# Performance work log

Hardware: AMD Instinct MI355X
Metric: run time of the kernel (lower is better)

Reference implementation:

```python
import jax, jax.numpy as jnp
import numpy as np

B, D = 8192, 1024
LABEL_SMOOTHING = 0.1
EPS = 1e-7


def setup_inputs() -> dict:
    key = jax.random.key(0)
    k1, k2 = jax.random.split(key)
    # Poincare-ball points must have norm < 1; scale so ||x|| ~ 0.6
    sign_emb = jax.random.normal(k1, (B, D), dtype=jnp.float32) * 0.02
    text_emb = jax.random.normal(k2, (B, D), dtype=jnp.float32) * 0.02
    log_tau = jnp.float32(0.0)   # nn.Parameter(torch.tensor(0.0))
    margin = jnp.float32(0.3)    # nn.Parameter(torch.tensor(0.3))
    return {"sign_emb": sign_emb, "text_emb": text_emb,
            "log_tau": log_tau, "margin": margin}


def poincare_dist_matrix(x, y):
    # Closed form of PoincareBall(c=1).dist for all pairs, no (B,B,d) intermediate:
    # d(x,y) = arccosh(1 + 2||x-y||^2 / ((1-||x||^2)(1-||y||^2)))
    xx = jnp.sum(x * x, axis=-1)                      # (B,)
    yy = jnp.sum(y * y, axis=-1)                      # (B,)
    xy = jnp.einsum('id,jd->ij', x, y)                # (B,B) Gram matmul
    sq = jnp.maximum(xx[:, None] + yy[None, :] - 2.0 * xy, 0.0)
    denom = jnp.maximum((1.0 - xx)[:, None] * (1.0 - yy)[None, :], EPS)
    arg = 1.0 + 2.0 * sq / denom
    return jnp.arccosh(jnp.maximum(arg, 1.0 + EPS))   # (B,B)


def reference(sign_emb, text_emb, log_tau, margin):
    b = sign_emb.shape[0]
    geo_dist = poincare_dist_matrix(sign_emb, text_emb)           # (B,B)
    tau = jax.nn.sigmoid(log_tau) * 1.99 + 0.01
    is_negative = 1.0 - jnp.eye(b, dtype=geo_dist.dtype)
    scores = -geo_dist / tau + jnp.maximum(margin, 0.0) * is_negative
    # CrossEntropyLoss(label_smoothing) with labels = arange(B)
    logp = jax.nn.log_softmax(scores, axis=-1)
    nll = -jnp.diagonal(logp)                                     # (B,)
    smooth = -jnp.mean(logp, axis=-1)                             # (B,)
    loss = jnp.mean((1.0 - LABEL_SMOOTHING) * nll + LABEL_SMOOTHING * smooth)
    pos_dist = jnp.mean(jnp.diagonal(geo_dist))
    return loss, pos_dist, tau, jnp.maximum(margin, margin)  # margin reported as-is
```

## Files before the change

kernel.cpp:

```cpp
#include <hip/hip_runtime.h>
#include <hip/hip_bf16.h>
#include <stdint.h>

#define BN 8192
#define DK 1024
#define BKT 64
#define NKT (DK / BKT)
#define LSMOOTH 0.1f
#define EPSF 1e-7f
#define LN2F 0.69314718055994531f

typedef float f32x4 __attribute__((ext_vector_type(4)));
typedef int   i32x4 __attribute__((ext_vector_type(4)));

__global__ __launch_bounds__(256) void prep_kernel(
    const float* __restrict__ sign, const float* __restrict__ text,
    uint32_t* __restrict__ Aq, uint32_t* __restrict__ Bq,
    float* __restrict__ xx, float* __restrict__ yy, float* __restrict__ accums) {
  const int b = blockIdx.x;
  const int row = b & (BN - 1);
  const bool isB = b >= BN;
  const float4* src = (const float4*)((isB ? text : sign) + (size_t)row * DK);
  uint32_t* dst = (isB ? Bq : Aq) + (size_t)row * (DK / 4);
  const int t = threadIdx.x;
  if (b == 0 && t < 3) accums[t] = 0.f;
  float4 v = src[t];
  int q0 = __float2int_rn(fminf(fmaxf(v.x * 1024.f, -127.f), 127.f));
  int q1 = __float2int_rn(fminf(fmaxf(v.y * 1024.f, -127.f), 127.f));
  int q2 = __float2int_rn(fminf(fmaxf(v.z * 1024.f, -127.f), 127.f));
  int q3 = __float2int_rn(fminf(fmaxf(v.w * 1024.f, -127.f), 127.f));
  dst[t] = (uint32_t)(q0 & 0xFF) | ((uint32_t)(q1 & 0xFF) << 8) |
           ((uint32_t)(q2 & 0xFF) << 16) | ((uint32_t)(q3 & 0xFF) << 24);
  float ss = v.x * v.x + v.y * v.y + v.z * v.z + v.w * v.w;
  #pragma unroll
  for (int off = 32; off; off >>= 1) ss += __shfl_down(ss, off);
  __shared__ float red[4];
  if ((t & 63) == 0) red[t >> 6] = ss;
  __syncthreads();
  if (t == 0) (isB ? yy : xx)[row] = red[0] + red[1] + red[2] + red[3];
}

__global__ __launch_bounds__(512, 2) void gemm_fused(
    const uint8_t* __restrict__ Aq, const uint8_t* __restrict__ Bq,
    const float* __restrict__ xx, const float* __restrict__ yy,
    const float* __restrict__ p_log_tau, const float* __restrict__ p_margin,
    float* __restrict__ row_partial, float* __restrict__ accums) {
  __shared__ __align__(16) char lds[65536];

  const int tid = threadIdx.x;
  const int wave = tid >> 6, lane = tid & 63;
  const int l15 = lane & 15, g4 = lane >> 4;
  const int waveM = wave >> 2, waveN = wave & 3;
  const int bx = blockIdx.x, by = blockIdx.y;
  const int blockRow = by * 256, blockCol = bx * 256;

  const int srow = tid >> 2;
  const int schunk = (tid & 3) ^ ((srow >> 1) & 3);
  const uint8_t* aSrc = Aq + (size_t)(blockRow + srow) * DK + schunk * 16;
  const uint8_t* bSrc = Bq + (size_t)(blockCol + srow) * DK + schunk * 16;
  const int ldst = wave * 1024;

#define GLL(gp, lp) __builtin_amdgcn_global_load_lds(                                   \
      (const __attribute__((address_space(1))) void*)(gp),                             \
      (__attribute__((address_space(3))) void*)(lp), 16, 0, 0)
#define STAGE_A(kt, cb) do { char* b_ = lds + (cb);                                     \
    const uint8_t* s_ = aSrc + (kt) * BKT;                                              \
    GLL(s_, b_ + ldst); GLL(s_ + 128 * DK, b_ + 8192 + ldst); } while (0)
#define STAGE_B(kt, cb) do { char* b_ = lds + (cb) + 16384;                             \
    const uint8_t* s_ = bSrc + (kt) * BKT;                                              \
    GLL(s_, b_ + ldst); GLL(s_ + 128 * DK, b_ + 8192 + ldst); } while (0)
#define RD128(off) (*(const i32x4*)(lds + (off)))
#define BAR() do { __builtin_amdgcn_s_barrier(); asm volatile("" ::: "memory"); } while (0)
#define LGKM0() do { asm volatile("s_waitcnt lgkmcnt(0)" ::: "memory");                 \
                     __builtin_amdgcn_sched_barrier(0); } while (0)
#define MFMAI(a_, b_, c_) __builtin_amdgcn_mfma_i32_16x16x64_i8((a_), (b_), (c_), 0, 0, 0)

  i32x4 acc[8][4];
  #pragma unroll
  for (int m = 0; m < 8; ++m)
    #pragma unroll
    for (int n = 0; n < 4; ++n)
      acc[m][n] = (i32x4){0, 0, 0, 0};

  const int s2 = (l15 >> 1) & 3;
  const int co = ((g4 ^ s2) << 4);
  const int aRow = (waveM * 128 + l15) * 64;
  const int bRow = 16384 + (waveN * 64 + l15) * 64;

  i32x4 af[4], bf[4];

  STAGE_A(0, 0); STAGE_B(0, 0);
  asm volatile("s_waitcnt vmcnt(0)" ::: "memory");
  BAR();

  for (int t = 0; t < NKT; ++t) {
    const int cb = (t & 1) * 32768;
    const int nb = ((t + 1) & 1) * 32768;
    #pragma unroll
    for (int m = 0; m < 4; ++m) af[m] = RD128(cb + aRow + m * 1024 + co);
    #pragma unroll
    for (int n = 0; n < 2; ++n) bf[n] = RD128(cb + bRow + n * 1024 + co);
    if (t + 1 < NKT) STAGE_A(t + 1, nb);
    BAR(); LGKM0();
    __builtin_amdgcn_s_setprio(1);
    #pragma unroll
    for (int m = 0; m < 4; ++m)
      #pragma unroll
      for (int n = 0; n < 2; ++n)
        acc[m][n] = MFMAI(af[m], bf[n], acc[m][n]);
    __builtin_amdgcn_s_setprio(0);
    BAR();
    #pragma unroll
    for (int n = 2; n < 4; ++n) bf[n] = RD128(cb + bRow + n * 1024 + co);
    if (t + 1 < NKT) STAGE_B(t + 1, nb);
    BAR(); LGKM0();
    __builtin_amdgcn_s_setprio(1);
    #pragma unroll
    for (int m = 0; m < 4; ++m)
      #pragma unroll
      for (int n = 2; n < 4; ++n)
        acc[m][n] = MFMAI(af[m], bf[n], acc[m][n]);
    __builtin_amdgcn_s_setprio(0);
    BAR();
    #pragma unroll
    for (int m = 0; m < 4; ++m) af[m] = RD128(cb + aRow + (m + 4) * 1024 + co);
    BAR(); LGKM0();
    __builtin_amdgcn_s_setprio(1);
    #pragma unroll
    for (int m = 0; m < 4; ++m)
      #pragma unroll
      for (int n = 0; n < 2; ++n)
        acc[m + 4][n] = MFMAI(af[m], bf[n], acc[m + 4][n]);
    __builtin_amdgcn_s_setprio(0);
    BAR();
    __builtin_amdgcn_s_setprio(1);
    #pragma unroll
    for (int m = 0; m < 4; ++m)
      #pragma unroll
      for (int n = 2; n < 4; ++n)
        acc[m + 4][n] = MFMAI(af[m], bf[n], acc[m + 4][n]);
    __builtin_amdgcn_s_setprio(0);
    asm volatile("s_waitcnt vmcnt(0)" ::: "memory");
    BAR();
  }
#undef STAGE_A
#undef STAGE_B
#undef GLL
#undef RD128
#undef BAR
#undef LGKM0
#undef MFMAI

  const float lt = *p_log_tau;
  const float mg = *p_margin;
  const float marg = fmaxf(mg, 0.f);
  const float tau = 1.99f / (1.f + __expf(-lt)) + 0.01f;
  const float nl = -LN2F / tau;
  const float em = __expf(-marg);
  const bool diagblk = (bx == by);
  const float dq = 9.5367431640625e-07f;

  float yyj[4], rcpy[4]; int gj[4];
  #pragma unroll
  for (int n = 0; n < 4; ++n) {
    gj[n] = blockCol + waveN * 64 + n * 16 + l15;
    yyj[n] = yy[gj[n]];
    rcpy[n] = __builtin_amdgcn_rcpf(1.f - yyj[n]);
  }

  float dL = 0.f, dDiagL = 0.f;
  float* rsum = (float*)lds;

  #pragma unroll
  for (int m = 0; m < 8; ++m) {
    #pragma unroll
    for (int r = 0; r < 4; ++r) {
      const int gi = blockRow + waveM * 128 + m * 16 + g4 * 4 + r;
      const float xxi = xx[gi];
      const float p2 = 2.f * __builtin_amdgcn_rcpf(1.f - xxi);
      float e_acc = 0.f;
      #pragma unroll
      for (int n = 0; n < 4; ++n) {
        const float xy = (float)acc[m][n][r] * dq;
        const float sq = fmaxf(xxi + yyj[n] - 2.f * xy, 0.f);
        const float tt = sq * (p2 * rcpy[n]);
        const float s = __builtin_amdgcn_sqrtf(tt * (tt + 2.f));
        const float w = tt + 1.f + s;
        const float L2 = __log2f(fmaxf(w, 1.f + EPSF));
        float e = __expf(L2 * nl);
        dL += L2;
        if (diagblk && gi == gj[n]) { dDiagL += L2; e *= em; }
        e_acc += e;
      }
      e_acc += __shfl_xor(e_acc, 1);
      e_acc += __shfl_xor(e_acc, 2);
      e_acc += __shfl_xor(e_acc, 4);
      e_acc += __shfl_xor(e_acc, 8);
      if (l15 == 0) {
        const int rloc = waveM * 128 + m * 16 + g4 * 4 + r;
        rsum[rloc * 4 + waveN] = e_acc;
      }
    }
  }

  #pragma unroll
  for (int off = 32; off; off >>= 1) {
    dL += __shfl_down(dL, off);
    dDiagL += __shfl_down(dDiagL, off);
  }
  if (lane == 0) {
    atomicAdd(&accums[0], dL);
    if (diagblk) atomicAdd(&accums[1], dDiagL);
  }

  __syncthreads();
  if (tid < 256) {
    const float rs = rsum[tid * 4 + 0] + rsum[tid * 4 + 1] + rsum[tid * 4 + 2] + rsum[tid * 4 + 3];
    row_partial[(size_t)bx * BN + blockRow + tid] = rs;
  }
}

__global__ __launch_bounds__(256) void logsum_kernel(
    const float* __restrict__ row_partial, float* __restrict__ accums) {
  const int row = blockIdx.x * 256 + threadIdx.x;
  float s = 0.f;
  #pragma unroll
  for (int c = 0; c < 32; ++c) s += row_partial[(size_t)c * BN + row];
  float lsum = __logf(s);
  #pragma unroll
  for (int off = 32; off; off >>= 1) lsum += __shfl_down(lsum, off);
  __shared__ float red[4];
  if ((threadIdx.x & 63) == 0) red[threadIdx.x >> 6] = lsum;
  __syncthreads();
  if (threadIdx.x == 0)
    atomicAdd(&accums[2], red[0] + red[1] + red[2] + red[3]);
}

__global__ void final_kernel(
    const float* __restrict__ accums,
    const float* __restrict__ p_log_tau, const float* __restrict__ p_margin,
    float* __restrict__ out) {
  const float lt = *p_log_tau;
  const float mg = *p_margin;
  const float marg = fmaxf(mg, 0.f);
  const float tau = 1.99f / (1.f + __expf(-lt)) + 0.01f;
  const float C = marg;
  const float d_tot = accums[0] * LN2F;
  const float d_diag = accums[1] * LN2F;
  const float bf = (float)BN;
  const float mean_lse = accums[2] / bf + C;
  const float sum_scores = -d_tot / tau + marg * (bf * bf - bf);
  const float sum_diag_scores = -d_diag / tau;
  const float loss = mean_lse
                   - (1.f - LSMOOTH) * (sum_diag_scores / bf)
                   - LSMOOTH * (sum_scores / (bf * bf));
  out[0] = loss;
  out[1] = d_diag / bf;
  out[2] = tau;
  out[3] = mg;
}

extern "C" void kernel_launch(void* const* d_in, const int* in_sizes, int n_in,
                              void* d_out, int out_size, void* d_ws, size_t ws_size,
                              hipStream_t stream) {
  const float* sign = (const float*)d_in[0];
  const float* text = (const float*)d_in[1];
  const float* p_log_tau = (const float*)d_in[2];
  const float* p_margin = (const float*)d_in[3];
  float* out = (float*)d_out;

  char* ws = (char*)d_ws;
  uint8_t* Aq = (uint8_t*)ws;
  uint8_t* Bq = (uint8_t*)(ws + (size_t)BN * DK);
  float* xx = (float*)(ws + (size_t)BN * DK * 2);
  float* yy = xx + BN;
  float* row_partial = yy + BN;
  float* accums = row_partial + 32 * BN;

  prep_kernel<<<dim3(2 * BN), 256, 0, stream>>>(sign, text, (uint32_t*)Aq, (uint32_t*)Bq,
                                                xx, yy, accums);
  gemm_fused<<<dim3(BN / 256, BN / 256), 512, 0, stream>>>(
      Aq, Bq, xx, yy, p_log_tau, p_margin, row_partial, accums);
  logsum_kernel<<<dim3(BN / 256), 256, 0, stream>>>(row_partial, accums);
  final_kernel<<<1, 1, 0, stream>>>(accums, p_log_tau, p_margin, out);
}
```

Before: 192.4 us.

## Software-pipeline int8 GEMM loop with register prefetch and fewer barriers

The int8 MFMA main loop now issues both global-to-LDS stages for the next k-tile at the top of each iteration. It prefetches the next tile's A and B fragments into extra registers after a single barrier, and uses partial lgkmcnt waits instead of four full barriers per k-step. The aim is to overlap LDS reads and global loads with MFMA work and cut synchronisation stalls. Launch bounds drop from 2 to 1 block per CU so the extra fragment registers fit without spilling, at the cost of fewer resident waves to hide latency.

```diff
diff --git a/kernel.cpp b/kernel.cpp
--- a/kernel.cpp
+++ b/kernel.cpp
@@ -40,7 +40,7 @@
   if (t == 0) (isB ? yy : xx)[row] = red[0] + red[1] + red[2] + red[3];
 }
 
-__global__ __launch_bounds__(512, 2) void gemm_fused(
+__global__ __launch_bounds__(512, 1) void gemm_fused(
     const uint8_t* __restrict__ Aq, const uint8_t* __restrict__ Bq,
     const float* __restrict__ xx, const float* __restrict__ yy,
     const float* __restrict__ p_log_tau, const float* __restrict__ p_margin,
@@ -70,9 +70,7 @@
     const uint8_t* s_ = bSrc + (kt) * BKT;                                              \
     GLL(s_, b_ + ldst); GLL(s_ + 128 * DK, b_ + 8192 + ldst); } while (0)
 #define RD128(off) (*(const i32x4*)(lds + (off)))
-#define BAR() do { __builtin_amdgcn_s_barrier(); asm volatile("" ::: "memory"); } while (0)
-#define LGKM0() do { asm volatile("s_waitcnt lgkmcnt(0)" ::: "memory");                 \
-                     __builtin_amdgcn_sched_barrier(0); } while (0)
+#define FENCE() __builtin_amdgcn_sched_barrier(0)
 #define MFMAI(a_, b_, c_) __builtin_amdgcn_mfma_i32_16x16x64_i8((a_), (b_), (c_), 0, 0, 0)
 
   i32x4 acc[8][4];
@@ -87,68 +85,71 @@
   const int aRow = (waveM * 128 + l15) * 64;
   const int bRow = 16384 + (waveN * 64 + l15) * 64;
 
-  i32x4 af[4], bf[4];
+  i32x4 af[4], ah[4], bf[4], bfN[4];
 
   STAGE_A(0, 0); STAGE_B(0, 0);
   asm volatile("s_waitcnt vmcnt(0)" ::: "memory");
-  BAR();
+  __builtin_amdgcn_s_barrier();
+  asm volatile("" ::: "memory");
+  #pragma unroll
+  for (int m = 0; m < 4; ++m) af[m] = RD128(aRow + m * 1024 + co);
+  #pragma unroll
+  for (int n = 0; n < 4; ++n) bf[n] = RD128(bRow + n * 1024 + co);
 
   for (int t = 0; t < NKT; ++t) {
     const int cb = (t & 1) * 32768;
     const int nb = ((t + 1) & 1) * 32768;
-    #pragma unroll
-    for (int m = 0; m < 4; ++m) af[m] = RD128(cb + aRow + m * 1024 + co);
-    #pragma unroll
-    for (int n = 0; n < 2; ++n) bf[n] = RD128(cb + bRow + n * 1024 + co);
-    if (t + 1 < NKT) STAGE_A(t + 1, nb);
-    BAR(); LGKM0();
+    const bool more = (t + 1 < NKT);
+    if (more) { STAGE_A(t + 1, nb); STAGE_B(t + 1, nb); }
+    #pragma unroll
+    for (int m = 0; m < 4; ++m) ah[m] = RD128(cb + aRow + (m + 4) * 1024 + co);
+    FENCE();
+    asm volatile("s_waitcnt lgkmcnt(4)" ::: "memory");
+    FENCE();
     __builtin_amdgcn_s_setprio(1);
     #pragma unroll
     for (int m = 0; m < 4; ++m)
       #pragma unroll
-      for (int n = 0; n < 2; ++n)
+      for (int n = 0; n < 4; ++n)
         acc[m][n] = MFMAI(af[m], bf[n], acc[m][n]);
     __builtin_amdgcn_s_setprio(0);
-    BAR();
-    #pragma unroll
-    for (int n = 2; n < 4; ++n) bf[n] = RD128(cb + bRow + n * 1024 + co);
-    if (t + 1 < NKT) STAGE_B(t + 1, nb);
-    BAR(); LGKM0();
+    asm volatile("s_waitcnt lgkmcnt(0)" ::: "memory");
+    FENCE();
     __builtin_amdgcn_s_setprio(1);
     #pragma unroll
     for (int m = 0; m < 4; ++m)
       #pragma unroll
+      for (int n = 0; n < 2; ++n)
+        acc[m + 4][n] = MFMAI(ah[m], bf[n], acc[m + 4][n]);
+    __builtin_amdgcn_s_setprio(0);
+    if (more) {
+      asm volatile("s_waitcnt vmcnt(0)" ::: "memory");
+      __builtin_amdgcn_s_barrier();
+      asm volatile("" ::: "memory");
+      #pragma unroll
+      for (int m = 0; m < 4; ++m) af[m] = RD128(nb + aRow + m * 1024 + co);
+      #pragma unroll
+      for (int n = 0; n < 4; ++n) bfN[n] = RD128(nb + bRow + n * 1024 + co);
+      FENCE();
+    }
+    __builtin_amdgcn_s_setprio(1);
+    #pragma unroll
+    for (int m = 0; m < 4; ++m)
+      #pragma unroll
       for (int n = 2; n < 4; ++n)
-        acc[m][n] = MFMAI(af[m], bf[n], acc[m][n]);
+        acc[m + 4][n] = MFMAI(ah[m], bf[n], acc[m + 4][n]);
     __builtin_amdgcn_s_setprio(0);
-    BAR();
-    #pragma unroll
-    for (int m = 0; m < 4; ++m) af[m] = RD128(cb + aRow + (m + 4) * 1024 + co);
-    BAR(); LGKM0();
-    __builtin_amdgcn_s_setprio(1);
-    #pragma unroll
-    for (int m = 0; m < 4; ++m)
-      #pragma unroll
-      for (int n = 0; n < 2; ++n)
-        acc[m + 4][n] = MFMAI(af[m], bf[n], acc[m + 4][n]);
-    __builtin_amdgcn_s_setprio(0);
-    BAR();
-    __builtin_amdgcn_s_setprio(1);
-    #pragma unroll
-    for (int m = 0; m < 4; ++m)
-      #pragma unroll
-      for (int n = 2; n < 4; ++n)
-        acc[m + 4][n] = MFMAI(af[m], bf[n], acc[m + 4][n]);
-    __builtin_amdgcn_s_setprio(0);
-    asm volatile("s_waitcnt vmcnt(0)" ::: "memory");
-    BAR();
-  }
+    if (more) {
+      #pragma unroll
+      for (int n = 0; n < 4; ++n) bf[n] = bfN[n];
+    }
+  }
+  __syncthreads();
 #undef STAGE_A
 #undef STAGE_B
 #undef GLL
 #undef RD128
-#undef BAR
-#undef LGKM0
+#undef FENCE
 #undef MFMAI
 
   const float lt = *p_log_tau;
```

New measurement: 189.8 us. About the same (-1.4%).
